# Optimization experiments

Hardware: AMD Instinct MI355X
Metric: run time of the kernel (lower is better)

The kernel has to match this reference:

```python
import jax, jax.numpy as jnp
import numpy as np

N = 8192
D_IN = 128
D_OUT = 128


def setup_inputs() -> dict:
    key = jax.random.key(0)
    k1, k2, k3 = jax.random.split(key, 3)
    x = jax.random.normal(k1, (N, D_IN), dtype=jnp.float32)
    adj = jax.random.uniform(k2, (N, N), dtype=jnp.float32)  # dense adjacency / edge weights
    weight = jax.random.normal(k3, (D_IN, D_OUT), dtype=jnp.float32) * (1.0 / np.sqrt(D_IN))
    bias = jnp.zeros((D_OUT,), dtype=jnp.float32)
    return {"x": x, "adj": adj, "weight": weight, "bias": bias}


def gcn_norm(adj, add_self_loops=False):
    # symmetric normalization: D^{-1/2} A D^{-1/2}
    if add_self_loops:
        adj = adj + jnp.eye(adj.shape[0], dtype=adj.dtype)
    deg = adj.sum(axis=1)
    dinv = jnp.where(deg > 0, jax.lax.rsqrt(deg), 0.0)  # masked_fill(isinf, 0)
    return adj * dinv[:, None] * dinv[None, :]


def reference(x, adj, weight, bias):
    adj_n = gcn_norm(adj, add_self_loops=False)  # cached normalized adjacency
    h = x @ weight                               # [N, D_out] dense projection
    out = adj_n @ h + bias                       # neighborhood aggregation + bias
    return out
```

## Files before the change

kernel.cpp:

```cpp
#include <hip/hip_runtime.h>
#include <hip/hip_bf16.h>

#define NN 8192
#define DD 128

typedef __attribute__((ext_vector_type(4))) float f32x4;
typedef __attribute__((ext_vector_type(8))) short s16x8;
typedef __attribute__((ext_vector_type(4))) short s16x4;

__device__ inline short bfbits(float f) {
    unsigned u = __builtin_bit_cast(unsigned, f);
    u += 0x7fffu + ((u >> 16) & 1u);
    return (short)(u >> 16);
}

__device__ inline s16x4 cvt4(f32x4 a) {
    s16x4 r;
    r[0] = bfbits(a[0]); r[1] = bfbits(a[1]); r[2] = bfbits(a[2]); r[3] = bfbits(a[3]);
    return r;
}

__device__ inline s16x8 cvt8(f32x4 a, f32x4 b) {
    s16x8 r;
    r[0] = bfbits(a[0]); r[1] = bfbits(a[1]); r[2] = bfbits(a[2]); r[3] = bfbits(a[3]);
    r[4] = bfbits(b[0]); r[5] = bfbits(b[1]); r[6] = bfbits(b[2]); r[7] = bfbits(b[3]);
    return r;
}

__global__ __launch_bounds__(256) void deg_kernel(const float* __restrict__ adj,
                                                  float* __restrict__ dinv) {
    const int lane = threadIdx.x & 63;
    const int row  = (blockIdx.x << 2) + (threadIdx.x >> 6);
    const float* r = adj + (size_t)row * NN;

    f32x4 s = {0.f, 0.f, 0.f, 0.f};
    #pragma unroll 4
    for (int it = 0; it < 32; ++it) {
        f32x4 v = *(const f32x4*)(r + it * 256 + (lane << 2));
        s += v;
    }
    float sum = s[0] + s[1] + s[2] + s[3];
    #pragma unroll
    for (int off = 32; off; off >>= 1) sum += __shfl_xor(sum, off, 64);
    if (lane == 0) dinv[row] = (sum > 0.f) ? rsqrtf(sum) : 0.f;
}

#define WST 132
__global__ __launch_bounds__(256) void proj_kernel(const float* __restrict__ x,
                                                   const float* __restrict__ w,
                                                   const float* __restrict__ dinv,
                                                   unsigned short* __restrict__ h2f) {
    __shared__ short lds_w[128 * WST];
    const int tid  = threadIdx.x;
    const int lane = tid & 63;
    const int wave = tid >> 6;
    const int j0   = blockIdx.x << 4;
    const int n0   = wave << 5;
    const int r    = lane & 15;
    const int q    = lane >> 4;

    #pragma unroll
    for (int i = 0; i < 16; ++i) {
        int gi = i * 256 + tid;
        int k  = gi >> 5;
        int n4 = (gi & 31) << 2;
        f32x4 v = *(const f32x4*)(w + (size_t)k * DD + n4);
        *(s16x4*)&lds_w[k * WST + n4] = cvt4(v);
    }
    __syncthreads();

    const float* xp = x + (size_t)(j0 + r) * DD + (q << 3);

    f32x4 acc0 = {0.f, 0.f, 0.f, 0.f};
    f32x4 acc1 = {0.f, 0.f, 0.f, 0.f};

    #pragma unroll
    for (int k = 0; k < DD; k += 32) {
        f32x4 a0 = *(const f32x4*)(xp + k);
        f32x4 a1 = *(const f32x4*)(xp + k + 4);
        s16x8 af = cvt8(a0, a1);

        const int kb = k + (q << 3);
        s16x8 b0, b1;
        #pragma unroll
        for (int jj = 0; jj < 8; ++jj) {
            b0[jj] = lds_w[(kb + jj) * WST + n0 + r];
            b1[jj] = lds_w[(kb + jj) * WST + n0 + 16 + r];
        }
        acc0 = __builtin_amdgcn_mfma_f32_16x16x32_bf16(af, b0, acc0, 0, 0, 0);
        acc1 = __builtin_amdgcn_mfma_f32_16x16x32_bf16(af, b1, acc1, 0, 0, 0);
    }

    #pragma unroll
    for (int rr = 0; rr < 4; ++rr) {
        const int j = j0 + (q << 2) + rr;
        const float dv = dinv[j];
        const int kg = j >> 5, qp = (j >> 3) & 3, jj = j & 7;
        #pragma unroll
        for (int half = 0; half < 2; ++half) {
            const int n = n0 + half * 16 + r;
            const int f = n >> 4;
            const int lanep = qp * 16 + (n & 15);
            const float v = (half ? acc1[rr] : acc0[rr]) * dv;
            h2f[((((size_t)f << 8) + kg) << 6 | lanep) * 8 + jj] = (unsigned short)bfbits(v);
        }
    }
}

template <int KSPLIT>
__global__ __launch_bounds__(256, 4) void agg_kernel(const float* __restrict__ adj,
                                                     const unsigned short* __restrict__ h2f,
                                                     const float* __restrict__ dinv,
                                                     const float* __restrict__ bias,
                                                     float* __restrict__ dst) {
    constexpr int KS    = NN / KSPLIT;
    constexpr int TILES = KS / 128;
    __shared__ short lds_a[2][16 * 16 * 8];

    const int tid  = threadIdx.x;
    const int lane = tid & 63;
    const int wave = tid >> 6;
    const int r    = lane & 15;
    const int q    = lane >> 4;
    const int m0   = blockIdx.x << 4;
    const int k0   = blockIdx.y * KS;

    const int row0 = tid >> 5;
    const int off0 = (tid & 31) << 2;
    const int cd   = (tid & 31) >> 1;
    const int hh   = tid & 1;
    const int so0  = ((row0 << 4) + (cd ^ row0)) * 8 + hh * 4;
    const int so1  = (((8 + row0) << 4) + (cd ^ (8 + row0))) * 8 + hh * 4;

    const float* ap0 = adj + (size_t)(m0 + row0) * NN + k0 + off0;
    const float* ap1 = adj + (size_t)(m0 + 8 + row0) * NN + k0 + off0;

    const unsigned short* bb0 = h2f + (((size_t)(wave * 2)     * 256 + (k0 >> 5)) * 64 + lane) * 8;
    const unsigned short* bb1 = h2f + (((size_t)(wave * 2 + 1) * 256 + (k0 >> 5)) * 64 + lane) * 8;

    f32x4 acc0 = {0.f, 0.f, 0.f, 0.f};
    f32x4 acc1 = {0.f, 0.f, 0.f, 0.f};

    {
        f32x4 v0 = *(const f32x4*)(ap0);
        f32x4 v1 = *(const f32x4*)(ap1);
        *(s16x4*)&lds_a[0][so0] = cvt4(v0);
        *(s16x4*)&lds_a[0][so1] = cvt4(v1);
    }
    __syncthreads();

    for (int t = 0; t < TILES; ++t) {
        const short* lcur = lds_a[t & 1];
        short* lnxt = (short*)lds_a[(t + 1) & 1];

        s16x8 br0[4], br1[4];
        #pragma unroll
        for (int s = 0; s < 4; ++s) {
            br0[s] = *(const s16x8*)(bb0 + (size_t)(t * 4 + s) * 512);
            br1[s] = *(const s16x8*)(bb1 + (size_t)(t * 4 + s) * 512);
        }
        f32x4 v0, v1;
        if (t + 1 < TILES) {
            v0 = *(const f32x4*)(ap0 + (t + 1) * 128);
            v1 = *(const f32x4*)(ap1 + (t + 1) * 128);
        }
        #pragma unroll
        for (int s = 0; s < 4; ++s) {
            const int slot = (r << 4) + (((s << 2) + q) ^ r);
            s16x8 af = *(const s16x8*)(lcur + slot * 8);
            acc0 = __builtin_amdgcn_mfma_f32_16x16x32_bf16(af, br0[s], acc0, 0, 0, 0);
            acc1 = __builtin_amdgcn_mfma_f32_16x16x32_bf16(af, br1[s], acc1, 0, 0, 0);
        }
        if (t + 1 < TILES) {
            *(s16x4*)(lnxt + so0) = cvt4(v0);
            *(s16x4*)(lnxt + so1) = cvt4(v1);
        }
        __syncthreads();
    }

    #pragma unroll
    for (int rr = 0; rr < 4; ++rr) {
        const int m = m0 + (q << 2) + rr;
        const int n = (wave << 5) + r;
        if (KSPLIT == 1) {
            const float dv = dinv[m];
            dst[(size_t)m * DD + n]      = acc0[rr] * dv + bias[n];
            dst[(size_t)m * DD + n + 16] = acc1[rr] * dv + bias[n + 16];
        } else {
            float* p = dst + (size_t)blockIdx.y * NN * DD;
            p[(size_t)m * DD + n]      = acc0[rr];
            p[(size_t)m * DD + n + 16] = acc1[rr];
        }
    }
}

__global__ __launch_bounds__(256) void reduce_kernel(const float* __restrict__ part,
                                                     const float* __restrict__ dinv,
                                                     const float* __restrict__ bias,
                                                     float* __restrict__ out) {
    const int idx = blockIdx.x * 256 + threadIdx.x;
    const f32x4 a = ((const f32x4*)part)[idx];
    const f32x4 b = ((const f32x4*)part)[idx + NN * DD / 4];
    const float dv = dinv[idx >> 5];
    const f32x4 bi = *(const f32x4*)(bias + ((idx & 31) << 2));
    f32x4 s = a + b;
    f32x4 o;
    o[0] = s[0] * dv + bi[0]; o[1] = s[1] * dv + bi[1];
    o[2] = s[2] * dv + bi[2]; o[3] = s[3] * dv + bi[3];
    ((f32x4*)out)[idx] = o;
}

extern "C" void kernel_launch(void* const* d_in, const int* in_sizes, int n_in,
                              void* d_out, int out_size, void* d_ws, size_t ws_size,
                              hipStream_t stream) {
    const float* x    = (const float*)d_in[0];
    const float* adj  = (const float*)d_in[1];
    const float* w    = (const float*)d_in[2];
    const float* bias = (const float*)d_in[3];
    float* out = (float*)d_out;

    float* dinv = (float*)d_ws;
    unsigned short* h2f = (unsigned short*)((char*)d_ws + 32 * 1024);
    float* part = (float*)((char*)d_ws + 32 * 1024 + 2 * 1024 * 1024);
    const size_t need2 = 32 * 1024 + 2 * 1024 * 1024 + (size_t)2 * NN * DD * sizeof(float);

    deg_kernel<<<NN / 4, 256, 0, stream>>>(adj, dinv);
    proj_kernel<<<NN / 16, 256, 0, stream>>>(x, w, dinv, h2f);

    if (ws_size >= need2) {
        agg_kernel<2><<<dim3(NN / 16, 2), 256, 0, stream>>>(adj, h2f, dinv, bias, part);
        reduce_kernel<<<NN * DD / 4 / 256, 256, 0, stream>>>(part, dinv, bias, out);
    } else {
        agg_kernel<1><<<dim3(NN / 16, 1), 256, 0, stream>>>(adj, h2f, dinv, bias, out);
    }
}
```

Measured before the change: 439.1 us.

## Fuse degree pass with bf16 adjacency conversion; aggregate from pre-swizzled bf16 copy

A new prep kernel reads the fp32 adjacency once, computing row degrees and writing a bf16, MFMA-swizzled copy, while the same launch runs the projection and stores unscaled fp32 results. A scale kernel then applies dinv and converts to bf16. Aggregation reads the half-size bf16 copy straight into LDS with global_load_lds, so it no longer reads and converts fp32 adjacency in registers. In exchange it writes and rereads 128 MB of workspace and adds an extra launch, with the old path kept as a fallback when workspace is small.

```diff
diff --git a/kernel.cpp b/kernel.cpp
--- a/kernel.cpp
+++ b/kernel.cpp
@@ -27,131 +27,164 @@
     return r;
 }
 
-__global__ __launch_bounds__(256) void deg_kernel(const float* __restrict__ adj,
-                                                  float* __restrict__ dinv) {
-    const int lane = threadIdx.x & 63;
-    const int row  = (blockIdx.x << 2) + (threadIdx.x >> 6);
-    const float* r = adj + (size_t)row * NN;
-
-    f32x4 s = {0.f, 0.f, 0.f, 0.f};
-    #pragma unroll 4
-    for (int it = 0; it < 32; ++it) {
-        f32x4 v = *(const f32x4*)(r + it * 256 + (lane << 2));
-        s += v;
-    }
-    float sum = s[0] + s[1] + s[2] + s[3];
-    #pragma unroll
-    for (int off = 32; off; off >>= 1) sum += __shfl_xor(sum, off, 64);
-    if (lane == 0) dinv[row] = (sum > 0.f) ? rsqrtf(sum) : 0.f;
-}
-
 #define WST 132
-__global__ __launch_bounds__(256) void proj_kernel(const float* __restrict__ x,
-                                                   const float* __restrict__ w,
-                                                   const float* __restrict__ dinv,
-                                                   unsigned short* __restrict__ h2f) {
+
+__global__ __launch_bounds__(512, 2) void prep_kernel(const float* __restrict__ adj,
+                                                      const float* __restrict__ x,
+                                                      const float* __restrict__ w,
+                                                      float* __restrict__ dinv,
+                                                      unsigned short* __restrict__ adjc,
+                                                      float* __restrict__ hU) {
     __shared__ short lds_w[128 * WST];
-    const int tid  = threadIdx.x;
-    const int lane = tid & 63;
-    const int wave = tid >> 6;
-    const int j0   = blockIdx.x << 4;
-    const int n0   = wave << 5;
-    const int r    = lane & 15;
-    const int q    = lane >> 4;
-
-    #pragma unroll
-    for (int i = 0; i < 16; ++i) {
-        int gi = i * 256 + tid;
-        int k  = gi >> 5;
-        int n4 = (gi & 31) << 2;
-        f32x4 v = *(const f32x4*)(w + (size_t)k * DD + n4);
-        *(s16x4*)&lds_w[k * WST + n4] = cvt4(v);
-    }
-    __syncthreads();
-
-    const float* xp = x + (size_t)(j0 + r) * DD + (q << 3);
-
-    f32x4 acc0 = {0.f, 0.f, 0.f, 0.f};
-    f32x4 acc1 = {0.f, 0.f, 0.f, 0.f};
-
-    #pragma unroll
-    for (int k = 0; k < DD; k += 32) {
-        f32x4 a0 = *(const f32x4*)(xp + k);
-        f32x4 a1 = *(const f32x4*)(xp + k + 4);
-        s16x8 af = cvt8(a0, a1);
-
-        const int kb = k + (q << 3);
-        s16x8 b0, b1;
-        #pragma unroll
-        for (int jj = 0; jj < 8; ++jj) {
-            b0[jj] = lds_w[(kb + jj) * WST + n0 + r];
-            b1[jj] = lds_w[(kb + jj) * WST + n0 + 16 + r];
-        }
-        acc0 = __builtin_amdgcn_mfma_f32_16x16x32_bf16(af, b0, acc0, 0, 0, 0);
-        acc1 = __builtin_amdgcn_mfma_f32_16x16x32_bf16(af, b1, acc1, 0, 0, 0);
-    }
-
-    #pragma unroll
-    for (int rr = 0; rr < 4; ++rr) {
-        const int j = j0 + (q << 2) + rr;
-        const float dv = dinv[j];
-        const int kg = j >> 5, qp = (j >> 3) & 3, jj = j & 7;
-        #pragma unroll
-        for (int half = 0; half < 2; ++half) {
-            const int n = n0 + half * 16 + r;
-            const int f = n >> 4;
-            const int lanep = qp * 16 + (n & 15);
-            const float v = (half ? acc1[rr] : acc0[rr]) * dv;
-            h2f[((((size_t)f << 8) + kg) << 6 | lanep) * 8 + jj] = (unsigned short)bfbits(v);
-        }
-    }
-}
-
-template <int KSPLIT>
-__global__ __launch_bounds__(256, 4) void agg_kernel(const float* __restrict__ adj,
-                                                     const unsigned short* __restrict__ h2f,
-                                                     const float* __restrict__ dinv,
-                                                     const float* __restrict__ bias,
-                                                     float* __restrict__ dst) {
-    constexpr int KS    = NN / KSPLIT;
-    constexpr int TILES = KS / 128;
-    __shared__ short lds_a[2][16 * 16 * 8];
-
+    const int tid = threadIdx.x;
+    const int grp = blockIdx.x >> 4;
+    const int sub = blockIdx.x & 15;
+
+    if (sub < 8) {
+        const int mb   = grp * 8 + sub;
+        const int row0 = tid >> 5;
+        const int off0 = (tid & 31) << 2;
+        const int cd   = (tid & 31) >> 1;
+        const int hh   = tid & 1;
+        const int so0  = ((row0 << 4) + (cd ^ row0)) * 8 + hh * 4;
+        const int so1  = (((16 + row0) << 4) + (cd ^ row0)) * 8 + hh * 4;
+
+        const float* ap0 = adj + (size_t)(mb * 32 + row0) * NN + off0;
+        const float* ap1 = ap0 + (size_t)16 * NN;
+        unsigned short* cb = adjc + (size_t)mb * (64 * 4096);
+
+        f32x4 s0 = {0.f, 0.f, 0.f, 0.f};
+        f32x4 s1 = {0.f, 0.f, 0.f, 0.f};
+        #pragma unroll 4
+        for (int t = 0; t < 64; ++t) {
+            f32x4 v0 = *(const f32x4*)(ap0 + t * 128);
+            f32x4 v1 = *(const f32x4*)(ap1 + t * 128);
+            s0 += v0; s1 += v1;
+            *(s16x4*)(cb + (size_t)t * 4096 + so0) = cvt4(v0);
+            *(s16x4*)(cb + (size_t)t * 4096 + so1) = cvt4(v1);
+        }
+        float r0 = s0[0] + s0[1] + s0[2] + s0[3];
+        float r1 = s1[0] + s1[1] + s1[2] + s1[3];
+        #pragma unroll
+        for (int off = 16; off; off >>= 1) {
+            r0 += __shfl_xor(r0, off, 32);
+            r1 += __shfl_xor(r1, off, 32);
+        }
+        if ((tid & 31) == 0) {
+            dinv[mb * 32 + row0]      = (r0 > 0.f) ? rsqrtf(r0) : 0.f;
+            dinv[mb * 32 + 16 + row0] = (r1 > 0.f) ? rsqrtf(r1) : 0.f;
+        }
+    } else {
+        const int pb   = grp * 8 + (sub - 8);
+        const int lane = tid & 63;
+        const int wave = tid >> 6;
+        const int r    = lane & 15;
+        const int q    = lane >> 4;
+        const int j0   = pb * 32 + (wave >> 2) * 16;
+        const int n0   = (wave & 3) << 5;
+
+        #pragma unroll
+        for (int i = 0; i < 8; ++i) {
+            int gi = i * 512 + tid;
+            int k  = gi >> 5;
+            int n4 = (gi & 31) << 2;
+            f32x4 v = *(const f32x4*)(w + (size_t)k * DD + n4);
+            *(s16x4*)&lds_w[k * WST + n4] = cvt4(v);
+        }
+        __syncthreads();
+
+        const float* xp = x + (size_t)(j0 + r) * DD + (q << 3);
+        f32x4 acc0 = {0.f, 0.f, 0.f, 0.f};
+        f32x4 acc1 = {0.f, 0.f, 0.f, 0.f};
+
+        #pragma unroll
+        for (int k = 0; k < DD; k += 32) {
+            f32x4 a0 = *(const f32x4*)(xp + k);
+            f32x4 a1 = *(const f32x4*)(xp + k + 4);
+            s16x8 af = cvt8(a0, a1);
+            const int kb = k + (q << 3);
+            s16x8 b0, b1;
+            #pragma unroll
+            for (int jj = 0; jj < 8; ++jj) {
+                b0[jj] = lds_w[(kb + jj) * WST + n0 + r];
+                b1[jj] = lds_w[(kb + jj) * WST + n0 + 16 + r];
+            }
+            acc0 = __builtin_amdgcn_mfma_f32_16x16x32_bf16(af, b0, acc0, 0, 0, 0);
+            acc1 = __builtin_amdgcn_mfma_f32_16x16x32_bf16(af, b1, acc1, 0, 0, 0);
+        }
+
+        #pragma unroll
+        for (int rr = 0; rr < 4; ++rr) {
+            const int j  = j0 + (q << 2) + rr;
+            const int kg = j >> 5, qp = (j >> 3) & 3, jj = j & 7;
+            #pragma unroll
+            for (int half = 0; half < 2; ++half) {
+                const int n = n0 + half * 16 + r;
+                const int f = n >> 4;
+                const int lanep = qp * 16 + (n & 15);
+                hU[(((size_t)((f << 8) | kg) << 6) | lanep) * 8 + jj] =
+                    (half ? acc1[rr] : acc0[rr]);
+            }
+        }
+    }
+}
+
+__global__ __launch_bounds__(256) void scale_kernel(const float* __restrict__ hU,
+                                                    const float* __restrict__ dinv,
+                                                    unsigned short* __restrict__ h2f) {
+    const int s  = blockIdx.x * 256 + threadIdx.x;
+    const int kg = (s >> 6) & 255;
+    const int qp = (s >> 4) & 3;
+    const int j0 = (kg << 5) + (qp << 3);
+    f32x4 a  = *(const f32x4*)(hU + (size_t)s * 8);
+    f32x4 b  = *(const f32x4*)(hU + (size_t)s * 8 + 4);
+    f32x4 d0 = *(const f32x4*)(dinv + j0);
+    f32x4 d1 = *(const f32x4*)(dinv + j0 + 4);
+    s16x8 o;
+    o[0] = bfbits(a[0] * d0[0]); o[1] = bfbits(a[1] * d0[1]);
+    o[2] = bfbits(a[2] * d0[2]); o[3] = bfbits(a[3] * d0[3]);
+    o[4] = bfbits(b[0] * d1[0]); o[5] = bfbits(b[1] * d1[1]);
+    o[6] = bfbits(b[2] * d1[2]); o[7] = bfbits(b[3] * d1[3]);
+    *(s16x8*)(h2f + (size_t)s * 8) = o;
+}
+
+__device__ inline void stage_tile(const unsigned short* __restrict__ src,
+                                  short* lds_base, int tid) {
+    const __attribute__((address_space(1))) unsigned int* g =
+        (const __attribute__((address_space(1))) unsigned int*)src + ((size_t)tid << 2);
+    __attribute__((address_space(3))) unsigned int* l =
+        (__attribute__((address_space(3))) unsigned int*)(lds_base + ((tid >> 6) << 9));
+    __builtin_amdgcn_global_load_lds(g, l, 16, 0, 0);
+}
+
+__global__ __launch_bounds__(512, 4) void agg2_kernel(const unsigned short* __restrict__ adjc,
+                                                      const unsigned short* __restrict__ h2f,
+                                                      float* __restrict__ part) {
+    __shared__ __align__(16) short lds_a[2][4096];
     const int tid  = threadIdx.x;
     const int lane = tid & 63;
     const int wave = tid >> 6;
     const int r    = lane & 15;
     const int q    = lane >> 4;
-    const int m0   = blockIdx.x << 4;
-    const int k0   = blockIdx.y * KS;
-
-    const int row0 = tid >> 5;
-    const int off0 = (tid & 31) << 2;
-    const int cd   = (tid & 31) >> 1;
-    const int hh   = tid & 1;
-    const int so0  = ((row0 << 4) + (cd ^ row0)) * 8 + hh * 4;
-    const int so1  = (((8 + row0) << 4) + (cd ^ (8 + row0))) * 8 + hh * 4;
-
-    const float* ap0 = adj + (size_t)(m0 + row0) * NN + k0 + off0;
-    const float* ap1 = adj + (size_t)(m0 + 8 + row0) * NN + k0 + off0;
-
-    const unsigned short* bb0 = h2f + (((size_t)(wave * 2)     * 256 + (k0 >> 5)) * 64 + lane) * 8;
-    const unsigned short* bb1 = h2f + (((size_t)(wave * 2 + 1) * 256 + (k0 >> 5)) * 64 + lane) * 8;
+    const int w4   = wave & 3;
+    const int half = wave >> 2;
+    const int mb   = blockIdx.x;
+    const int by   = blockIdx.y;
+
+    const unsigned short* asrc = adjc + (size_t)mb * (64 * 4096) + (size_t)by * (32 * 4096);
+    const unsigned short* bb0 =
+        h2f + (((size_t)(w4 * 2)     * 256 + (size_t)by * 128) * 64 + lane) * 8;
+    const unsigned short* bb1 =
+        h2f + (((size_t)(w4 * 2 + 1) * 256 + (size_t)by * 128) * 64 + lane) * 8;
 
     f32x4 acc0 = {0.f, 0.f, 0.f, 0.f};
     f32x4 acc1 = {0.f, 0.f, 0.f, 0.f};
 
-    {
-        f32x4 v0 = *(const f32x4*)(ap0);
-        f32x4 v1 = *(const f32x4*)(ap1);
-        *(s16x4*)&lds_a[0][so0] = cvt4(v0);
-        *(s16x4*)&lds_a[0][so1] = cvt4(v1);
-    }
+    stage_tile(asrc, lds_a[0], tid);
     __syncthreads();
 
-    for (int t = 0; t < TILES; ++t) {
+    for (int t = 0; t < 32; ++t) {
         const short* lcur = lds_a[t & 1];
-        short* lnxt = (short*)lds_a[(t + 1) & 1];
 
         s16x8 br0[4], br1[4];
         #pragma unroll
@@ -159,38 +192,25 @@
             br0[s] = *(const s16x8*)(bb0 + (size_t)(t * 4 + s) * 512);
             br1[s] = *(const s16x8*)(bb1 + (size_t)(t * 4 + s) * 512);
         }
-        f32x4 v0, v1;
-        if (t + 1 < TILES) {
-            v0 = *(const f32x4*)(ap0 + (t + 1) * 128);
-            v1 = *(const f32x4*)(ap1 + (t + 1) * 128);
-        }
+        if (t + 1 < 32) stage_tile(asrc + (size_t)(t + 1) * 4096, lds_a[(t + 1) & 1], tid);
+
         #pragma unroll
         for (int s = 0; s < 4; ++s) {
-            const int slot = (r << 4) + (((s << 2) + q) ^ r);
+            const int slot = (((half << 4) | r) << 4) + (((s << 2) + q) ^ r);
             s16x8 af = *(const s16x8*)(lcur + slot * 8);
             acc0 = __builtin_amdgcn_mfma_f32_16x16x32_bf16(af, br0[s], acc0, 0, 0, 0);
             acc1 = __builtin_amdgcn_mfma_f32_16x16x32_bf16(af, br1[s], acc1, 0, 0, 0);
         }
-        if (t + 1 < TILES) {
-            *(s16x4*)(lnxt + so0) = cvt4(v0);
-            *(s16x4*)(lnxt + so1) = cvt4(v1);
-        }
         __syncthreads();
     }
 
     #pragma unroll
     for (int rr = 0; rr < 4; ++rr) {
-        const int m = m0 + (q << 2) + rr;
-        const int n = (wave << 5) + r;
-        if (KSPLIT == 1) {
-            const float dv = dinv[m];
-            dst[(size_t)m * DD + n]      = acc0[rr] * dv + bias[n];
-            dst[(size_t)m * DD + n + 16] = acc1[rr] * dv + bias[n + 16];
-        } else {
-            float* p = dst + (size_t)blockIdx.y * NN * DD;
-            p[(size_t)m * DD + n]      = acc0[rr];
-            p[(size_t)m * DD + n + 16] = acc1[rr];
-        }
+        const int m = (mb << 5) + (half << 4) + (q << 2) + rr;
+        const int n = (w4 << 5) + r;
+        float* p = part + (size_t)by * (NN * DD);
+        p[(size_t)m * DD + n]      = acc0[rr];
+        p[(size_t)m * DD + n + 16] = acc1[rr];
     }
 }
 
@@ -210,6 +230,150 @@
     ((f32x4*)out)[idx] = o;
 }
 
+__global__ __launch_bounds__(256) void deg_kernel(const float* __restrict__ adj,
+                                                  float* __restrict__ dinv) {
+    const int lane = threadIdx.x & 63;
+    const int row  = (blockIdx.x << 2) + (threadIdx.x >> 6);
+    const float* r = adj + (size_t)row * NN;
+    f32x4 s = {0.f, 0.f, 0.f, 0.f};
+    #pragma unroll 4
+    for (int it = 0; it < 32; ++it) {
+        f32x4 v = *(const f32x4*)(r + it * 256 + (lane << 2));
+        s += v;
+    }
+    float sum = s[0] + s[1] + s[2] + s[3];
+    #pragma unroll
+    for (int off = 32; off; off >>= 1) sum += __shfl_xor(sum, off, 64);
+    if (lane == 0) dinv[row] = (sum > 0.f) ? rsqrtf(sum) : 0.f;
+}
+
+__global__ __launch_bounds__(256) void proj_kernel(const float* __restrict__ x,
+                                                   const float* __restrict__ w,
+                                                   const float* __restrict__ dinv,
+                                                   unsigned short* __restrict__ h2f) {
+    __shared__ short lds_w[128 * WST];
+    const int tid  = threadIdx.x;
+    const int lane = tid & 63;
+    const int wave = tid >> 6;
+    const int j0   = blockIdx.x << 4;
+    const int n0   = wave << 5;
+    const int r    = lane & 15;
+    const int q    = lane >> 4;
+    #pragma unroll
+    for (int i = 0; i < 16; ++i) {
+        int gi = i * 256 + tid;
+        int k  = gi >> 5;
+        int n4 = (gi & 31) << 2;
+        f32x4 v = *(const f32x4*)(w + (size_t)k * DD + n4);
+        *(s16x4*)&lds_w[k * WST + n4] = cvt4(v);
+    }
+    __syncthreads();
+    const float* xp = x + (size_t)(j0 + r) * DD + (q << 3);
+    f32x4 acc0 = {0.f, 0.f, 0.f, 0.f};
+    f32x4 acc1 = {0.f, 0.f, 0.f, 0.f};
+    #pragma unroll
+    for (int k = 0; k < DD; k += 32) {
+        f32x4 a0 = *(const f32x4*)(xp + k);
+        f32x4 a1 = *(const f32x4*)(xp + k + 4);
+        s16x8 af = cvt8(a0, a1);
+        const int kb = k + (q << 3);
+        s16x8 b0, b1;
+        #pragma unroll
+        for (int jj = 0; jj < 8; ++jj) {
+            b0[jj] = lds_w[(kb + jj) * WST + n0 + r];
+            b1[jj] = lds_w[(kb + jj) * WST + n0 + 16 + r];
+        }
+        acc0 = __builtin_amdgcn_mfma_f32_16x16x32_bf16(af, b0, acc0, 0, 0, 0);
+        acc1 = __builtin_amdgcn_mfma_f32_16x16x32_bf16(af, b1, acc1, 0, 0, 0);
+    }
+    #pragma unroll
+    for (int rr = 0; rr < 4; ++rr) {
+        const int j = j0 + (q << 2) + rr;
+        const float dv = dinv[j];
+        const int kg = j >> 5, qp = (j >> 3) & 3, jj = j & 7;
+        #pragma unroll
+        for (int half = 0; half < 2; ++half) {
+            const int n = n0 + half * 16 + r;
+            const int f = n >> 4;
+            const int lanep = qp * 16 + (n & 15);
+            const float v = (half ? acc1[rr] : acc0[rr]) * dv;
+            h2f[((((size_t)f << 8) + kg) << 6 | lanep) * 8 + jj] = (unsigned short)bfbits(v);
+        }
+    }
+}
+
+template <int KSPLIT>
+__global__ __launch_bounds__(256, 4) void agg_kernel(const float* __restrict__ adj,
+                                                     const unsigned short* __restrict__ h2f,
+                                                     const float* __restrict__ dinv,
+                                                     const float* __restrict__ bias,
+                                                     float* __restrict__ dst) {
+    constexpr int KS    = NN / KSPLIT;
+    constexpr int TILES = KS / 128;
+    __shared__ short lds_a[2][16 * 16 * 8];
+    const int tid  = threadIdx.x;
+    const int lane = tid & 63;
+    const int wave = tid >> 6;
+    const int r    = lane & 15;
+    const int q    = lane >> 4;
+    const int m0   = blockIdx.x << 4;
+    const int k0   = blockIdx.y * KS;
+    const int row0 = tid >> 5;
+    const int off0 = (tid & 31) << 2;
+    const int cd   = (tid & 31) >> 1;
+    const int hh   = tid & 1;
+    const int so0  = ((row0 << 4) + (cd ^ row0)) * 8 + hh * 4;
+    const int so1  = (((8 + row0) << 4) + (cd ^ (8 + row0))) * 8 + hh * 4;
+    const float* ap0 = adj + (size_t)(m0 + row0) * NN + k0 + off0;
+    const float* ap1 = adj + (size_t)(m0 + 8 + row0) * NN + k0 + off0;
+    const unsigned short* bb0 = h2f + (((size_t)(wave * 2)     * 256 + (k0 >> 5)) * 64 + lane) * 8;
+    const unsigned short* bb1 = h2f + (((size_t)(wave * 2 + 1) * 256 + (k0 >> 5)) * 64 + lane) * 8;
+    f32x4 acc0 = {0.f, 0.f, 0.f, 0.f};
+    f32x4 acc1 = {0.f, 0.f, 0.f, 0.f};
+    {
+        f32x4 v0 = *(const f32x4*)(ap0);
+        f32x4 v1 = *(const f32x4*)(ap1);
+        *(s16x4*)&lds_a[0][so0] = cvt4(v0);
+        *(s16x4*)&lds_a[0][so1] = cvt4(v1);
+    }
+    __syncthreads();
+    for (int t = 0; t < TILES; ++t) {
+        const short* lcur = lds_a[t & 1];
+        short* lnxt = (short*)lds_a[(t + 1) & 1];
+        s16x8 br0[4], br1[4];
+        #pragma unroll
+        for (int s = 0; s < 4; ++s) {
+            br0[s] = *(const s16x8*)(bb0 + (size_t)(t * 4 + s) * 512);
+            br1[s] = *(const s16x8*)(bb1 + (size_t)(t * 4 + s) * 512);
+        }
+        f32x4 v0, v1;
+        if (t + 1 < TILES) {
+            v0 = *(const f32x4*)(ap0 + (t + 1) * 128);
+            v1 = *(const f32x4*)(ap1 + (t + 1) * 128);
+        }
+        #pragma unroll
+        for (int s = 0; s < 4; ++s) {
+            const int slot = (r << 4) + (((s << 2) + q) ^ r);
+            s16x8 af = *(const s16x8*)(lcur + slot * 8);
+            acc0 = __builtin_amdgcn_mfma_f32_16x16x32_bf16(af, br0[s], acc0, 0, 0, 0);
+            acc1 = __builtin_amdgcn_mfma_f32_16x16x32_bf16(af, br1[s], acc1, 0, 0, 0);
+        }
+        if (t + 1 < TILES) {
+            *(s16x4*)(lnxt + so0) = cvt4(v0);
+            *(s16x4*)(lnxt + so1) = cvt4(v1);
+        }
+        __syncthreads();
+    }
+    #pragma unroll
+    for (int rr = 0; rr < 4; ++rr) {
+        const int m = m0 + (q << 2) + rr;
+        const int n = (wave << 5) + r;
+        const float dv = dinv[m];
+        dst[(size_t)m * DD + n]      = acc0[rr] * dv + bias[n];
+        dst[(size_t)m * DD + n + 16] = acc1[rr] * dv + bias[n + 16];
+    }
+}
+
 extern "C" void kernel_launch(void* const* d_in, const int* in_sizes, int n_in,
                               void* d_out, int out_size, void* d_ws, size_t ws_size,
                               hipStream_t stream) {
@@ -219,18 +383,21 @@
     const float* bias = (const float*)d_in[3];
     float* out = (float*)d_out;
 
-    float* dinv = (float*)d_ws;
+    float* dinv         = (float*)d_ws;
     unsigned short* h2f = (unsigned short*)((char*)d_ws + 32 * 1024);
-    float* part = (float*)((char*)d_ws + 32 * 1024 + 2 * 1024 * 1024);
-    const size_t need2 = 32 * 1024 + 2 * 1024 * 1024 + (size_t)2 * NN * DD * sizeof(float);
-
-    deg_kernel<<<NN / 4, 256, 0, stream>>>(adj, dinv);
-    proj_kernel<<<NN / 16, 256, 0, stream>>>(x, w, dinv, h2f);
-
-    if (ws_size >= need2) {
-        agg_kernel<2><<<dim3(NN / 16, 2), 256, 0, stream>>>(adj, h2f, dinv, bias, part);
+    float* hU           = (float*)((char*)d_ws + 32 * 1024 + 2 * 1024 * 1024);
+    unsigned short* adjc = (unsigned short*)((char*)d_ws + 32 * 1024 + 6 * 1024 * 1024);
+    float* part         = (float*)((char*)adjc + 134217728ull);
+    const size_t need_new = 32 * 1024 + 6 * 1024 * 1024 + 134217728ull + 8 * 1024 * 1024;
+
+    if (ws_size >= need_new) {
+        prep_kernel<<<512, 512, 0, stream>>>(adj, x, w, dinv, adjc, hU);
+        scale_kernel<<<512, 256, 0, stream>>>(hU, dinv, h2f);
+        agg2_kernel<<<dim3(256, 2), 512, 0, stream>>>(adjc, h2f, part);
         reduce_kernel<<<NN * DD / 4 / 256, 256, 0, stream>>>(part, dinv, bias, out);
     } else {
+        deg_kernel<<<NN / 4, 256, 0, stream>>>(adj, dinv);
+        proj_kernel<<<NN / 16, 256, 0, stream>>>(x, w, dinv, h2f);
         agg_kernel<1><<<dim3(NN / 16, 1), 256, 0, stream>>>(adj, h2f, dinv, bias, out);
     }
 }
```

Result: slower. 457.3 us (+4.1%).

## Merge degree and projection into one launch; double agg K-step per iteration

Applied to the files above, without the earlier changes.

Degree reduction and the x@W projection now run in a single interleaved launch, 4 degree blocks for every projection block. The projection writes unscaled fp32 to a staging buffer, and a new scale kernel applies dinv and converts to bf16. This removes the serial dependency between the two prep kernels so they can overlap. The aggregation loop also now processes 256 K per iteration with a double set of LDS tiles, halving barriers and putting more loads in flight. The cost is an extra 4 MB fp32 round trip, one more launch, and higher register and LDS use in the aggregation kernel.

```diff
diff --git a/kernel.cpp b/kernel.cpp
--- a/kernel.cpp
+++ b/kernel.cpp
@@ -27,84 +27,106 @@
     return r;
 }
 
-__global__ __launch_bounds__(256) void deg_kernel(const float* __restrict__ adj,
-                                                  float* __restrict__ dinv) {
-    const int lane = threadIdx.x & 63;
-    const int row  = (blockIdx.x << 2) + (threadIdx.x >> 6);
-    const float* r = adj + (size_t)row * NN;
-
-    f32x4 s = {0.f, 0.f, 0.f, 0.f};
-    #pragma unroll 4
-    for (int it = 0; it < 32; ++it) {
-        f32x4 v = *(const f32x4*)(r + it * 256 + (lane << 2));
-        s += v;
-    }
-    float sum = s[0] + s[1] + s[2] + s[3];
-    #pragma unroll
-    for (int off = 32; off; off >>= 1) sum += __shfl_xor(sum, off, 64);
-    if (lane == 0) dinv[row] = (sum > 0.f) ? rsqrtf(sum) : 0.f;
-}
-
 #define WST 132
-__global__ __launch_bounds__(256) void proj_kernel(const float* __restrict__ x,
-                                                   const float* __restrict__ w,
-                                                   const float* __restrict__ dinv,
-                                                   unsigned short* __restrict__ h2f) {
+
+__global__ __launch_bounds__(256) void prep2_kernel(const float* __restrict__ adj,
+                                                    const float* __restrict__ x,
+                                                    const float* __restrict__ w,
+                                                    float* __restrict__ dinv,
+                                                    float* __restrict__ hU) {
     __shared__ short lds_w[128 * WST];
-    const int tid  = threadIdx.x;
-    const int lane = tid & 63;
-    const int wave = tid >> 6;
-    const int j0   = blockIdx.x << 4;
-    const int n0   = wave << 5;
-    const int r    = lane & 15;
-    const int q    = lane >> 4;
-
-    #pragma unroll
-    for (int i = 0; i < 16; ++i) {
-        int gi = i * 256 + tid;
-        int k  = gi >> 5;
-        int n4 = (gi & 31) << 2;
-        f32x4 v = *(const f32x4*)(w + (size_t)k * DD + n4);
-        *(s16x4*)&lds_w[k * WST + n4] = cvt4(v);
-    }
-    __syncthreads();
-
-    const float* xp = x + (size_t)(j0 + r) * DD + (q << 3);
-
-    f32x4 acc0 = {0.f, 0.f, 0.f, 0.f};
-    f32x4 acc1 = {0.f, 0.f, 0.f, 0.f};
-
-    #pragma unroll
-    for (int k = 0; k < DD; k += 32) {
-        f32x4 a0 = *(const f32x4*)(xp + k);
-        f32x4 a1 = *(const f32x4*)(xp + k + 4);
-        s16x8 af = cvt8(a0, a1);
-
-        const int kb = k + (q << 3);
-        s16x8 b0, b1;
-        #pragma unroll
-        for (int jj = 0; jj < 8; ++jj) {
-            b0[jj] = lds_w[(kb + jj) * WST + n0 + r];
-            b1[jj] = lds_w[(kb + jj) * WST + n0 + 16 + r];
-        }
-        acc0 = __builtin_amdgcn_mfma_f32_16x16x32_bf16(af, b0, acc0, 0, 0, 0);
-        acc1 = __builtin_amdgcn_mfma_f32_16x16x32_bf16(af, b1, acc1, 0, 0, 0);
-    }
-
-    #pragma unroll
-    for (int rr = 0; rr < 4; ++rr) {
-        const int j = j0 + (q << 2) + rr;
-        const float dv = dinv[j];
-        const int kg = j >> 5, qp = (j >> 3) & 3, jj = j & 7;
-        #pragma unroll
-        for (int half = 0; half < 2; ++half) {
-            const int n = n0 + half * 16 + r;
-            const int f = n >> 4;
-            const int lanep = qp * 16 + (n & 15);
-            const float v = (half ? acc1[rr] : acc0[rr]) * dv;
-            h2f[((((size_t)f << 8) + kg) << 6 | lanep) * 8 + jj] = (unsigned short)bfbits(v);
-        }
-    }
+    const int tid = threadIdx.x;
+    const int sub = blockIdx.x % 5;
+    const int grp = blockIdx.x / 5;
+
+    if (sub < 4) {
+        const int db   = grp * 4 + sub;
+        const int lane = tid & 63;
+        const int row  = (db << 2) + (tid >> 6);
+        const float* r = adj + (size_t)row * NN;
+
+        f32x4 s = {0.f, 0.f, 0.f, 0.f};
+        #pragma unroll 4
+        for (int it = 0; it < 32; ++it) {
+            f32x4 v = *(const f32x4*)(r + it * 256 + (lane << 2));
+            s += v;
+        }
+        float sum = s[0] + s[1] + s[2] + s[3];
+        #pragma unroll
+        for (int off = 32; off; off >>= 1) sum += __shfl_xor(sum, off, 64);
+        if (lane == 0) dinv[row] = (sum > 0.f) ? rsqrtf(sum) : 0.f;
+    } else {
+        const int pb   = grp;
+        const int lane = tid & 63;
+        const int wave = tid >> 6;
+        const int j0   = pb << 4;
+        const int n0   = wave << 5;
+        const int r    = lane & 15;
+        const int q    = lane >> 4;
+
+        #pragma unroll
+        for (int i = 0; i < 16; ++i) {
+            int gi = i * 256 + tid;
+            int k  = gi >> 5;
+            int n4 = (gi & 31) << 2;
+            f32x4 v = *(const f32x4*)(w + (size_t)k * DD + n4);
+            *(s16x4*)&lds_w[k * WST + n4] = cvt4(v);
+        }
+        __syncthreads();
+
+        const float* xp = x + (size_t)(j0 + r) * DD + (q << 3);
+        f32x4 acc0 = {0.f, 0.f, 0.f, 0.f};
+        f32x4 acc1 = {0.f, 0.f, 0.f, 0.f};
+
+        #pragma unroll
+        for (int k = 0; k < DD; k += 32) {
+            f32x4 a0 = *(const f32x4*)(xp + k);
+            f32x4 a1 = *(const f32x4*)(xp + k + 4);
+            s16x8 af = cvt8(a0, a1);
+            const int kb = k + (q << 3);
+            s16x8 b0, b1;
+            #pragma unroll
+            for (int jj = 0; jj < 8; ++jj) {
+                b0[jj] = lds_w[(kb + jj) * WST + n0 + r];
+                b1[jj] = lds_w[(kb + jj) * WST + n0 + 16 + r];
+            }
+            acc0 = __builtin_amdgcn_mfma_f32_16x16x32_bf16(af, b0, acc0, 0, 0, 0);
+            acc1 = __builtin_amdgcn_mfma_f32_16x16x32_bf16(af, b1, acc1, 0, 0, 0);
+        }
+
+        #pragma unroll
+        for (int rr = 0; rr < 4; ++rr) {
+            const int j  = j0 + (q << 2) + rr;
+            const int kg = j >> 5, qp = (j >> 3) & 3, jj = j & 7;
+            #pragma unroll
+            for (int half = 0; half < 2; ++half) {
+                const int n = n0 + half * 16 + r;
+                const int f = n >> 4;
+                const int lanep = qp * 16 + (n & 15);
+                hU[(((size_t)((f << 8) | kg) << 6) | lanep) * 8 + jj] =
+                    (half ? acc1[rr] : acc0[rr]);
+            }
+        }
+    }
+}
+
+__global__ __launch_bounds__(256) void scale_kernel(const float* __restrict__ hU,
+                                                    const float* __restrict__ dinv,
+                                                    unsigned short* __restrict__ h2f) {
+    const int s  = blockIdx.x * 256 + threadIdx.x;
+    const int kg = (s >> 6) & 255;
+    const int qp = (s >> 4) & 3;
+    const int j0 = (kg << 5) + (qp << 3);
+    f32x4 a  = *(const f32x4*)(hU + (size_t)s * 8);
+    f32x4 b  = *(const f32x4*)(hU + (size_t)s * 8 + 4);
+    f32x4 d0 = *(const f32x4*)(dinv + j0);
+    f32x4 d1 = *(const f32x4*)(dinv + j0 + 4);
+    s16x8 o;
+    o[0] = bfbits(a[0] * d0[0]); o[1] = bfbits(a[1] * d0[1]);
+    o[2] = bfbits(a[2] * d0[2]); o[3] = bfbits(a[3] * d0[3]);
+    o[4] = bfbits(b[0] * d1[0]); o[5] = bfbits(b[1] * d1[1]);
+    o[6] = bfbits(b[2] * d1[2]); o[7] = bfbits(b[3] * d1[3]);
+    *(s16x8*)(h2f + (size_t)s * 8) = o;
 }
 
 template <int KSPLIT>
@@ -114,8 +136,8 @@
                                                      const float* __restrict__ bias,
                                                      float* __restrict__ dst) {
     constexpr int KS    = NN / KSPLIT;
-    constexpr int TILES = KS / 128;
-    __shared__ short lds_a[2][16 * 16 * 8];
+    constexpr int ITERS = KS / 256;
+    __shared__ short lds_a[2][2][16 * 16 * 8];
 
     const int tid  = threadIdx.x;
     const int lane = tid & 63;
@@ -142,38 +164,55 @@
     f32x4 acc1 = {0.f, 0.f, 0.f, 0.f};
 
     {
-        f32x4 v0 = *(const f32x4*)(ap0);
-        f32x4 v1 = *(const f32x4*)(ap1);
-        *(s16x4*)&lds_a[0][so0] = cvt4(v0);
-        *(s16x4*)&lds_a[0][so1] = cvt4(v1);
+        f32x4 a0 = *(const f32x4*)(ap0);
+        f32x4 a1 = *(const f32x4*)(ap1);
+        f32x4 b0 = *(const f32x4*)(ap0 + 128);
+        f32x4 b1 = *(const f32x4*)(ap1 + 128);
+        *(s16x4*)&lds_a[0][0][so0] = cvt4(a0);
+        *(s16x4*)&lds_a[0][0][so1] = cvt4(a1);
+        *(s16x4*)&lds_a[0][1][so0] = cvt4(b0);
+        *(s16x4*)&lds_a[0][1][so1] = cvt4(b1);
     }
     __syncthreads();
 
-    for (int t = 0; t < TILES; ++t) {
-        const short* lcur = lds_a[t & 1];
-        short* lnxt = (short*)lds_a[(t + 1) & 1];
-
-        s16x8 br0[4], br1[4];
-        #pragma unroll
-        for (int s = 0; s < 4; ++s) {
-            br0[s] = *(const s16x8*)(bb0 + (size_t)(t * 4 + s) * 512);
-            br1[s] = *(const s16x8*)(bb1 + (size_t)(t * 4 + s) * 512);
-        }
-        f32x4 v0, v1;
-        if (t + 1 < TILES) {
-            v0 = *(const f32x4*)(ap0 + (t + 1) * 128);
-            v1 = *(const f32x4*)(ap1 + (t + 1) * 128);
+    for (int t = 0; t < ITERS; ++t) {
+        const short* lc0 = lds_a[t & 1][0];
+        const short* lc1 = lds_a[t & 1][1];
+
+        s16x8 br0[8], br1[8];
+        #pragma unroll
+        for (int s = 0; s < 8; ++s) {
+            br0[s] = *(const s16x8*)(bb0 + (size_t)(t * 8 + s) * 512);
+            br1[s] = *(const s16x8*)(bb1 + (size_t)(t * 8 + s) * 512);
+        }
+        f32x4 v0a, v1a, v0b, v1b;
+        if (t + 1 < ITERS) {
+            v0a = *(const f32x4*)(ap0 + (t + 1) * 256);
+            v1a = *(const f32x4*)(ap1 + (t + 1) * 256);
+            v0b = *(const f32x4*)(ap0 + (t + 1) * 256 + 128);
+            v1b = *(const f32x4*)(ap1 + (t + 1) * 256 + 128);
         }
         #pragma unroll
         for (int s = 0; s < 4; ++s) {
             const int slot = (r << 4) + (((s << 2) + q) ^ r);
-            s16x8 af = *(const s16x8*)(lcur + slot * 8);
+            s16x8 af = *(const s16x8*)(lc0 + slot * 8);
             acc0 = __builtin_amdgcn_mfma_f32_16x16x32_bf16(af, br0[s], acc0, 0, 0, 0);
             acc1 = __builtin_amdgcn_mfma_f32_16x16x32_bf16(af, br1[s], acc1, 0, 0, 0);
         }
-        if (t + 1 < TILES) {
-            *(s16x4*)(lnxt + so0) = cvt4(v0);
-            *(s16x4*)(lnxt + so1) = cvt4(v1);
+        #pragma unroll
+        for (int s = 0; s < 4; ++s) {
+            const int slot = (r << 4) + (((s << 2) + q) ^ r);
+            s16x8 af = *(const s16x8*)(lc1 + slot * 8);
+            acc0 = __builtin_amdgcn_mfma_f32_16x16x32_bf16(af, br0[4 + s], acc0, 0, 0, 0);
+            acc1 = __builtin_amdgcn_mfma_f32_16x16x32_bf16(af, br1[4 + s], acc1, 0, 0, 0);
+        }
+        if (t + 1 < ITERS) {
+            short* ln0 = (short*)lds_a[(t + 1) & 1][0];
+            short* ln1 = (short*)lds_a[(t + 1) & 1][1];
+            *(s16x4*)(ln0 + so0) = cvt4(v0a);
+            *(s16x4*)(ln0 + so1) = cvt4(v1a);
+            *(s16x4*)(ln1 + so0) = cvt4(v0b);
+            *(s16x4*)(ln1 + so1) = cvt4(v1b);
         }
         __syncthreads();
     }
@@ -210,6 +249,78 @@
     ((f32x4*)out)[idx] = o;
 }
 
+__global__ __launch_bounds__(256) void deg_kernel(const float* __restrict__ adj,
+                                                  float* __restrict__ dinv) {
+    const int lane = threadIdx.x & 63;
+    const int row  = (blockIdx.x << 2) + (threadIdx.x >> 6);
+    const float* r = adj + (size_t)row * NN;
+    f32x4 s = {0.f, 0.f, 0.f, 0.f};
+    #pragma unroll 4
+    for (int it = 0; it < 32; ++it) {
+        f32x4 v = *(const f32x4*)(r + it * 256 + (lane << 2));
+        s += v;
+    }
+    float sum = s[0] + s[1] + s[2] + s[3];
+    #pragma unroll
+    for (int off = 32; off; off >>= 1) sum += __shfl_xor(sum, off, 64);
+    if (lane == 0) dinv[row] = (sum > 0.f) ? rsqrtf(sum) : 0.f;
+}
+
+__global__ __launch_bounds__(256) void proj_kernel(const float* __restrict__ x,
+                                                   const float* __restrict__ w,
+                                                   const float* __restrict__ dinv,
+                                                   unsigned short* __restrict__ h2f) {
+    __shared__ short lds_w[128 * WST];
+    const int tid  = threadIdx.x;
+    const int lane = tid & 63;
+    const int wave = tid >> 6;
+    const int j0   = blockIdx.x << 4;
+    const int n0   = wave << 5;
+    const int r    = lane & 15;
+    const int q    = lane >> 4;
+    #pragma unroll
+    for (int i = 0; i < 16; ++i) {
+        int gi = i * 256 + tid;
+        int k  = gi >> 5;
+        int n4 = (gi & 31) << 2;
+        f32x4 v = *(const f32x4*)(w + (size_t)k * DD + n4);
+        *(s16x4*)&lds_w[k * WST + n4] = cvt4(v);
+    }
+    __syncthreads();
+    const float* xp = x + (size_t)(j0 + r) * DD + (q << 3);
+    f32x4 acc0 = {0.f, 0.f, 0.f, 0.f};
+    f32x4 acc1 = {0.f, 0.f, 0.f, 0.f};
+    #pragma unroll
+    for (int k = 0; k < DD; k += 32) {
+        f32x4 a0 = *(const f32x4*)(xp + k);
+        f32x4 a1 = *(const f32x4*)(xp + k + 4);
+        s16x8 af = cvt8(a0, a1);
+        const int kb = k + (q << 3);
+        s16x8 b0, b1;
+        #pragma unroll
+        for (int jj = 0; jj < 8; ++jj) {
+            b0[jj] = lds_w[(kb + jj) * WST + n0 + r];
+            b1[jj] = lds_w[(kb + jj) * WST + n0 + 16 + r];
+        }
+        acc0 = __builtin_amdgcn_mfma_f32_16x16x32_bf16(af, b0, acc0, 0, 0, 0);
+        acc1 = __builtin_amdgcn_mfma_f32_16x16x32_bf16(af, b1, acc1, 0, 0, 0);
+    }
+    #pragma unroll
+    for (int rr = 0; rr < 4; ++rr) {
+        const int j = j0 + (q << 2) + rr;
+        const float dv = dinv[j];
+        const int kg = j >> 5, qp = (j >> 3) & 3, jj = j & 7;
+        #pragma unroll
+        for (int half = 0; half < 2; ++half) {
+            const int n = n0 + half * 16 + r;
+            const int f = n >> 4;
+            const int lanep = qp * 16 + (n & 15);
+            const float v = (half ? acc1[rr] : acc0[rr]) * dv;
+            h2f[((((size_t)f << 8) + kg) << 6 | lanep) * 8 + jj] = (unsigned short)bfbits(v);
+        }
+    }
+}
+
 extern "C" void kernel_launch(void* const* d_in, const int* in_sizes, int n_in,
                               void* d_out, int out_size, void* d_ws, size_t ws_size,
                               hipStream_t stream) {
@@ -219,18 +330,20 @@
     const float* bias = (const float*)d_in[3];
     float* out = (float*)d_out;
 
-    float* dinv = (float*)d_ws;
+    float* dinv         = (float*)d_ws;
     unsigned short* h2f = (unsigned short*)((char*)d_ws + 32 * 1024);
-    float* part = (float*)((char*)d_ws + 32 * 1024 + 2 * 1024 * 1024);
-    const size_t need2 = 32 * 1024 + 2 * 1024 * 1024 + (size_t)2 * NN * DD * sizeof(float);
-
-    deg_kernel<<<NN / 4, 256, 0, stream>>>(adj, dinv);
-    proj_kernel<<<NN / 16, 256, 0, stream>>>(x, w, dinv, h2f);
+    float* hU           = (float*)((char*)d_ws + 32 * 1024 + 2 * 1024 * 1024);
+    float* part         = (float*)((char*)d_ws + 32 * 1024 + 6 * 1024 * 1024);
+    const size_t need2 = 32 * 1024 + 6 * 1024 * 1024 + (size_t)2 * NN * DD * sizeof(float);
 
     if (ws_size >= need2) {
+        prep2_kernel<<<2560, 256, 0, stream>>>(adj, x, w, dinv, hU);
+        scale_kernel<<<512, 256, 0, stream>>>(hU, dinv, h2f);
         agg_kernel<2><<<dim3(NN / 16, 2), 256, 0, stream>>>(adj, h2f, dinv, bias, part);
         reduce_kernel<<<NN * DD / 4 / 256, 256, 0, stream>>>(part, dinv, bias, out);
     } else {
+        deg_kernel<<<NN / 4, 256, 0, stream>>>(adj, dinv);
+        proj_kernel<<<NN / 16, 256, 0, stream>>>(x, w, dinv, h2f);
         agg_kernel<1><<<dim3(NN / 16, 1), 256, 0, stream>>>(adj, h2f, dinv, bias, out);
     }
 }
```

Result: slower. 451.1 us (+2.7%).

## Use 32-row aggregation tiles with 4-way K split and 4-way reduce

Applied to the files above, without the earlier changes.

Adds an aggregation kernel where each block covers 32 output rows instead of 16. Each h fragment loaded into registers now feeds twice as many MFMAs, which halves the B-operand traffic per row. The K dimension is split four ways so the grid keeps the same block count, and a new reduce kernel sums four partial buffers and applies the dinv scale and bias. The cost is a larger workspace and twice as many partial-sum bytes written and read back, and the new path runs only if the workspace is big enough.

```diff
diff --git a/kernel.cpp b/kernel.cpp
--- a/kernel.cpp
+++ b/kernel.cpp
@@ -108,6 +108,105 @@
 }
 
 template <int KSPLIT>
+__global__ __launch_bounds__(256, 4) void agg32_kernel(const float* __restrict__ adj,
+                                                       const unsigned short* __restrict__ h2f,
+                                                       float* __restrict__ dst) {
+    constexpr int KS    = NN / KSPLIT;
+    constexpr int TILES = KS / 128;
+    __shared__ short lds_a[2][2][16 * 16 * 8];
+
+    const int tid  = threadIdx.x;
+    const int lane = tid & 63;
+    const int wave = tid >> 6;
+    const int r    = lane & 15;
+    const int q    = lane >> 4;
+    const int m0   = blockIdx.x << 5;
+    const int k0   = blockIdx.y * KS;
+
+    const int row0 = tid >> 5;
+    const int off0 = (tid & 31) << 2;
+    const int cd   = (tid & 31) >> 1;
+    const int hh   = tid & 1;
+    const int so0  = ((row0 << 4) + (cd ^ row0)) * 8 + hh * 4;
+    const int so1  = (((8 + row0) << 4) + (cd ^ (8 + row0))) * 8 + hh * 4;
+
+    const float* ap0 = adj + (size_t)(m0 + row0)      * NN + k0 + off0;
+    const float* ap1 = adj + (size_t)(m0 + 8 + row0)  * NN + k0 + off0;
+    const float* ap2 = adj + (size_t)(m0 + 16 + row0) * NN + k0 + off0;
+    const float* ap3 = adj + (size_t)(m0 + 24 + row0) * NN + k0 + off0;
+
+    const unsigned short* bb0 = h2f + (((size_t)(wave * 2)     * 256 + (k0 >> 5)) * 64 + lane) * 8;
+    const unsigned short* bb1 = h2f + (((size_t)(wave * 2 + 1) * 256 + (k0 >> 5)) * 64 + lane) * 8;
+
+    f32x4 acc00 = {0.f, 0.f, 0.f, 0.f};
+    f32x4 acc01 = {0.f, 0.f, 0.f, 0.f};
+    f32x4 acc10 = {0.f, 0.f, 0.f, 0.f};
+    f32x4 acc11 = {0.f, 0.f, 0.f, 0.f};
+
+    {
+        f32x4 v0 = *(const f32x4*)(ap0);
+        f32x4 v1 = *(const f32x4*)(ap1);
+        f32x4 v2 = *(const f32x4*)(ap2);
+        f32x4 v3 = *(const f32x4*)(ap3);
+        *(s16x4*)&lds_a[0][0][so0] = cvt4(v0);
+        *(s16x4*)&lds_a[0][0][so1] = cvt4(v1);
+        *(s16x4*)&lds_a[0][1][so0] = cvt4(v2);
+        *(s16x4*)&lds_a[0][1][so1] = cvt4(v3);
+    }
+    __syncthreads();
+
+    for (int t = 0; t < TILES; ++t) {
+        const short* lc0 = lds_a[t & 1][0];
+        const short* lc1 = lds_a[t & 1][1];
+
+        s16x8 br0[4], br1[4];
+        #pragma unroll
+        for (int s = 0; s < 4; ++s) {
+            br0[s] = *(const s16x8*)(bb0 + (size_t)(t * 4 + s) * 512);
+            br1[s] = *(const s16x8*)(bb1 + (size_t)(t * 4 + s) * 512);
+        }
+        f32x4 v0, v1, v2, v3;
+        if (t + 1 < TILES) {
+            v0 = *(const f32x4*)(ap0 + (t + 1) * 128);
+            v1 = *(const f32x4*)(ap1 + (t + 1) * 128);
+            v2 = *(const f32x4*)(ap2 + (t + 1) * 128);
+            v3 = *(const f32x4*)(ap3 + (t + 1) * 128);
+        }
+        #pragma unroll
+        for (int s = 0; s < 4; ++s) {
+            const int slot = (r << 4) + (((s << 2) + q) ^ r);
+            s16x8 afA = *(const s16x8*)(lc0 + slot * 8);
+            s16x8 afB = *(const s16x8*)(lc1 + slot * 8);
+            acc00 = __builtin_amdgcn_mfma_f32_16x16x32_bf16(afA, br0[s], acc00, 0, 0, 0);
+            acc01 = __builtin_amdgcn_mfma_f32_16x16x32_bf16(afA, br1[s], acc01, 0, 0, 0);
+            acc10 = __builtin_amdgcn_mfma_f32_16x16x32_bf16(afB, br0[s], acc10, 0, 0, 0);
+            acc11 = __builtin_amdgcn_mfma_f32_16x16x32_bf16(afB, br1[s], acc11, 0, 0, 0);
+        }
+        if (t + 1 < TILES) {
+            short* ln0 = (short*)lds_a[(t + 1) & 1][0];
+            short* ln1 = (short*)lds_a[(t + 1) & 1][1];
+            *(s16x4*)(ln0 + so0) = cvt4(v0);
+            *(s16x4*)(ln0 + so1) = cvt4(v1);
+            *(s16x4*)(ln1 + so0) = cvt4(v2);
+            *(s16x4*)(ln1 + so1) = cvt4(v3);
+        }
+        __syncthreads();
+    }
+
+    float* p = dst + (size_t)blockIdx.y * NN * DD;
+    #pragma unroll
+    for (int rr = 0; rr < 4; ++rr) {
+        const int mA = m0 + (q << 2) + rr;
+        const int mB = mA + 16;
+        const int n  = (wave << 5) + r;
+        p[(size_t)mA * DD + n]      = acc00[rr];
+        p[(size_t)mA * DD + n + 16] = acc01[rr];
+        p[(size_t)mB * DD + n]      = acc10[rr];
+        p[(size_t)mB * DD + n + 16] = acc11[rr];
+    }
+}
+
+template <int KSPLIT>
 __global__ __launch_bounds__(256, 4) void agg_kernel(const float* __restrict__ adj,
                                                      const unsigned short* __restrict__ h2f,
                                                      const float* __restrict__ dinv,
@@ -192,6 +291,24 @@
             p[(size_t)m * DD + n + 16] = acc1[rr];
         }
     }
+}
+
+__global__ __launch_bounds__(256) void reduce4_kernel(const float* __restrict__ part,
+                                                      const float* __restrict__ dinv,
+                                                      const float* __restrict__ bias,
+                                                      float* __restrict__ out) {
+    const int idx = blockIdx.x * 256 + threadIdx.x;
+    const f32x4 a = ((const f32x4*)part)[idx];
+    const f32x4 b = ((const f32x4*)part)[idx + NN * DD / 4];
+    const f32x4 c = ((const f32x4*)part)[idx + 2 * (NN * DD / 4)];
+    const f32x4 d = ((const f32x4*)part)[idx + 3 * (NN * DD / 4)];
+    const float dv = dinv[idx >> 5];
+    const f32x4 bi = *(const f32x4*)(bias + ((idx & 31) << 2));
+    f32x4 s = (a + b) + (c + d);
+    f32x4 o;
+    o[0] = s[0] * dv + bi[0]; o[1] = s[1] * dv + bi[1];
+    o[2] = s[2] * dv + bi[2]; o[3] = s[3] * dv + bi[3];
+    ((f32x4*)out)[idx] = o;
 }
 
 __global__ __launch_bounds__(256) void reduce_kernel(const float* __restrict__ part,
@@ -222,12 +339,17 @@
     float* dinv = (float*)d_ws;
     unsigned short* h2f = (unsigned short*)((char*)d_ws + 32 * 1024);
     float* part = (float*)((char*)d_ws + 32 * 1024 + 2 * 1024 * 1024);
-    const size_t need2 = 32 * 1024 + 2 * 1024 * 1024 + (size_t)2 * NN * DD * sizeof(float);
+    const size_t base  = 32 * 1024 + 2 * 1024 * 1024;
+    const size_t need4 = base + (size_t)4 * NN * DD * sizeof(float);
+    const size_t need2 = base + (size_t)2 * NN * DD * sizeof(float);
 
     deg_kernel<<<NN / 4, 256, 0, stream>>>(adj, dinv);
     proj_kernel<<<NN / 16, 256, 0, stream>>>(x, w, dinv, h2f);
 
-    if (ws_size >= need2) {
+    if (ws_size >= need4) {
+        agg32_kernel<4><<<dim3(NN / 32, 4), 256, 0, stream>>>(adj, h2f, part);
+        reduce4_kernel<<<NN * DD / 4 / 256, 256, 0, stream>>>(part, dinv, bias, out);
+    } else if (ws_size >= need2) {
         agg_kernel<2><<<dim3(NN / 16, 2), 256, 0, stream>>>(adj, h2f, dinv, bias, part);
         reduce_kernel<<<NN * DD / 4 / 256, 256, 0, stream>>>(part, dinv, bias, out);
     } else {
```

Result: faster. 425.6 us (-3.1%).
